# Performance work log

Hardware: AMD Instinct MI355X
Metric: run time of the kernel (lower is better)

Reference implementation:

```python
import jax, jax.numpy as jnp
import numpy as np

B, L = 1024, 4096        # cycles x timesteps
CC = 3                   # SC channels (SC[...,2:3] = nominal capacity)
XC = 2 + CC              # p_net input: [SOC, T, SC...]
# bounds from params['a123'] for (R_1, 1/R_1C_1, OCV-U, -M_H, K_H)
LB = jnp.array([0.005, 0.025, 0.1, 0.0, 0.002], dtype=jnp.float32)
UB = jnp.array([0.02, 0.07, 1.0, 0.055, 0.025], dtype=jnp.float32)


def setup_inputs() -> dict:
    key = jax.random.key(0)
    ks = jax.random.split(key, 10)
    t = jnp.broadcast_to(jnp.arange(L, dtype=jnp.float32), (B, L))  # monotone time
    I = 1.0 + 0.1 * jax.random.normal(ks[0], (B, L))  # current, bounded away from 0 (IR_estim divides by I)
    T = jax.random.normal(ks[1], (B, L))              # temperature
    dummy = jax.random.normal(ks[2], (B, L))          # unused column 3
    SOC = jax.random.uniform(ks[3], (B, L))
    X = jnp.stack([t, I, T, dummy, SOC], axis=-1)     # [B, L, 5]
    SC = jax.random.uniform(ks[4], (B, CC), minval=0.5, maxval=1.5)
    std = 0.1  # init_network_weights: normal(0, 0.1), zero bias
    pW1 = std * jax.random.normal(ks[5], (XC, 2 * XC))
    pb1 = jnp.zeros((2 * XC,), jnp.float32)
    pW2 = std * jax.random.normal(ks[6], (2 * XC, 5))
    pb2 = jnp.zeros((5,), jnp.float32)
    rW1 = std * jax.random.normal(ks[7], (XC, 1))
    rb1 = jnp.zeros((1,), jnp.float32)
    rW2 = std * jax.random.normal(ks[8], (1, 1))
    rb2 = jnp.zeros((1,), jnp.float32)
    return dict(X=X, SC=SC, pW1=pW1, pb1=pb1, pW2=pW2, pb2=pb2,
                rW1=rW1, rb1=rb1, rW2=rW2, rb2=rb2)


def reference(X, SC, pW1, pb1, pW2, pb2, rW1, rb1, rW2, rb2):
    t = X[..., 0:1]
    I = X[..., 1:2]
    T = X[..., 2:3]
    SOC = X[..., 4:]
    sc_b = jnp.broadcast_to(SC[:, None, :], (X.shape[0], X.shape[1], SC.shape[-1]))
    x = jnp.concatenate([SOC, T, sc_b], axis=-1)                 # [B, L, XC]
    p = jax.nn.softplus(x @ pW1 + pb1) @ pW2 + pb2               # [B, L, 5]
    theta = LB + (UB - LB) * jax.nn.sigmoid(0.01 * p)
    R_1 = theta[..., 0:1]
    RC_r = theta[..., 1:2]
    OCV_U = theta[..., 2:3]
    M_Hn = theta[..., 3:4]   # -M_H
    K_H = theta[..., 4:5]
    r = jax.nn.softplus(x[:, 0, :] @ rW1 + rb1) @ rW2 + rb2      # [B, 1]
    R_s_init = SC[..., 2:3] * (1.0 + r)
    U_H0 = jnp.zeros((X.shape[0], 1), X.dtype)
    U_10 = -OCV_U[:, 0, :] - U_H0 - I[:, 0, :] * R_s_init
    y0 = jnp.concatenate([U_H0, U_10], axis=-1)                  # [B, 2]

    dt = jnp.swapaxes(t[:, 1:, :] - t[:, :-1, :], 0, 1)          # [L-1, B, 1]
    tm = lambda a: jnp.swapaxes(a[:, :-1, :], 0, 1)              # step inputs use X_ode[:, i]
    scan_in = (dt, tm(I), tm(R_1), tm(RC_r), tm(M_Hn), tm(K_H))

    def step(y, inp):  # explicit Euler, IRODEFunc derivative
        dt_i, I_i, R1_i, RC_i, MH_i, KH_i = inp
        U_H = y[..., 0:1]
        U_1 = y[..., 1:2]
        dU_H = -KH_i * I_i * (-MH_i - U_H)
        dU_1 = RC_i * (R1_i * I_i - U_1)
        y = y + dt_i * jnp.concatenate([dU_H, dU_1], axis=-1)
        return y, y

    _, ys = jax.lax.scan(step, y0, scan_in)                      # [L-1, B, 2]
    voltages = jnp.concatenate([y0[None], ys], axis=0)           # [L, B, 2]
    voltages = jnp.swapaxes(voltages, 0, 1)                      # [B, L, 2]
    U_H = voltages[..., 0:1]
    U_1 = voltages[..., 1:2]
    IR_estim = jnp.nanmean((-OCV_U - U_H - U_1) / I, axis=-2)    # [B, 1]
    return IR_estim
```

## Files before the change

### kernel.cpp

```cpp
#include <hip/hip_runtime.h>

#define NB   1024
#define NL   4096
#define TPB  256
#define HALF 2048
#define SPT  8

#define WS_BASE 256
#define WS_PART 16640

typedef float v2f __attribute__((ext_vector_type(2)));

__device__ __forceinline__ float rfl(float x) {
    return __uint_as_float(__builtin_amdgcn_readfirstlane(__float_as_uint(x)));
}
__device__ __forceinline__ float fast_rcp(float x) { return __builtin_amdgcn_rcpf(x); }
__device__ __forceinline__ float fexp2(float x) { return __builtin_amdgcn_exp2f(x); }
__device__ __forceinline__ float flog2(float x) { return __builtin_amdgcn_logf(x); }

#define L2E 1.44269504088896340736f
#define LN2 0.69314718055994530942f

__global__ void __launch_bounds__(256) onenet_prep(
    const float* __restrict__ X,   const float* __restrict__ SC,
    const float* __restrict__ pW1, const float* __restrict__ pb1,
    const float* __restrict__ pW2, const float* __restrict__ pb2,
    const float* __restrict__ rW1, const float* __restrict__ rb1,
    const float* __restrict__ rW2, const float* __restrict__ rb2,
    float* __restrict__ ws)
{
    const int gid = blockIdx.x * 256 + threadIdx.x;
    if (gid < NB) {
        float sc0 = SC[gid * 3 + 0], sc1 = SC[gid * 3 + 1], sc2 = SC[gid * 3 + 2];
        float* bp = ws + WS_BASE + gid * 16;
#pragma unroll
        for (int j = 0; j < 10; ++j) {
            float base = fmaf(sc0, pW1[20 + j],
                         fmaf(sc1, pW1[30 + j],
                         fmaf(sc2, pW1[40 + j], pb1[j])));
            bp[j] = L2E * base;
        }
        const float* x0 = X + (size_t)gid * NL * 5;
        float T0 = x0[2], SOC0 = x0[4];
        float u = rb1[0];
        u = fmaf(SOC0, rW1[0], u);
        u = fmaf(T0,   rW1[1], u);
        u = fmaf(sc0,  rW1[2], u);
        u = fmaf(sc1,  rW1[3], u);
        u = fmaf(sc2,  rW1[4], u);
        float sp = LN2 * flog2(1.0f + fexp2(L2E * u));
        float r  = fmaf(sp, rW2[0], rb2[0]);
        bp[10] = sc2 * (1.0f + r);
    }
    if (blockIdx.x == 0 && threadIdx.x < 75) {
        const int t = threadIdx.x;
        const float LBv[5]   = {0.005f, 0.025f, 0.1f, 0.0f, 0.002f};
        const float UBLB[5]  = {0.015f, 0.045f, 0.9f, 0.055f, 0.023f};
        float v;
        if (t < 20) {
            v = L2E * pW1[t];
        } else if (t < 70) {
            int k = (t - 20) % 5;
            v = LN2 * 0.0025f * UBLB[k] * pW2[t - 20];
        } else {
            int k = t - 70;
            v = LBv[k] + UBLB[k] * fmaf(0.0025f, pb2[k], 0.5f);
        }
        ws[t] = v;
    }
}

__global__ void __launch_bounds__(TPB) onenet_main(
    const float* __restrict__ X, float* __restrict__ ws)
{
    const int bid  = blockIdx.x;
    const int row  = bid >> 1;
    const int half = bid & 1;
    const int tid  = threadIdx.x;
    const int lane = tid & 63;
    const int w    = tid >> 6;

    float W1S[10], W1T[10], BASE[10], V4[10];
    v2f V01[10], V23[10], AL01, AL23;
    float AL4;
#pragma unroll
    for (int j = 0; j < 10; ++j) W1S[j] = rfl(ws[j]);
#pragma unroll
    for (int j = 0; j < 10; ++j) W1T[j] = rfl(ws[10 + j]);
#pragma unroll
    for (int j = 0; j < 10; ++j) {
        V01[j].x = rfl(ws[20 + 5 * j + 0]);
        V01[j].y = rfl(ws[20 + 5 * j + 1]);
        V23[j].x = rfl(ws[20 + 5 * j + 2]);
        V23[j].y = rfl(ws[20 + 5 * j + 3]);
        V4[j]    = rfl(ws[20 + 5 * j + 4]);
    }
    AL01.x = rfl(ws[70]); AL01.y = rfl(ws[71]);
    AL23.x = rfl(ws[72]); AL23.y = rfl(ws[73]);
    AL4    = rfl(ws[74]);
    {
        const float* bp = ws + WS_BASE + row * 16;
#pragma unroll
        for (int j = 0; j < 10; ++j) BASE[j] = rfl(bp[j]);
    }

    const float* xp = X + ((size_t)row * NL + (size_t)(half * HALF + tid * SPT)) * 5;
    const bool lastthr = (half == 1) && (tid == TPB - 1);

    v2f a  = {1.f, 1.f}, b  = {0.f, 0.f};
    v2f cS = {0.f, 0.f}, dS = {0.f, 0.f};
    float oacc = 0.f, OCV0 = 0.f, I0 = 0.f;

#pragma unroll
    for (int ch = 0; ch < 2; ++ch) {
        float f[20];
#pragma unroll
        for (int q = 0; q < 5; ++q) {
            float4 v4 = reinterpret_cast<const float4*>(xp)[ch * 5 + q];
            f[4 * q + 0] = v4.x; f[4 * q + 1] = v4.y;
            f[4 * q + 2] = v4.z; f[4 * q + 3] = v4.w;
        }
        float tn = (ch == 0) ? xp[20] : (lastthr ? 0.f : xp[40]);

#pragma unroll
        for (int i = 0; i < 4; ++i) {
            float tt = f[5 * i + 0];
            float Ii = f[5 * i + 1];
            float Tt = f[5 * i + 2];
            float SS = f[5 * i + 4];
            float tnx = (i < 3) ? f[5 * i + 5] : tn;
            float dt  = tnx - tt;
            float inv = fast_rcp(Ii);

            v2f t01 = AL01, t23 = AL23;
            float t4 = AL4;
#pragma unroll
            for (int j = 0; j < 10; ++j) {
                float pre = fmaf(SS, W1S[j], fmaf(Tt, W1T[j], BASE[j]));
                float lam = flog2(1.0f + fexp2(pre));
                v2f lam2 = {lam, lam};
                t01 = lam2 * V01[j] + t01;
                t23 = lam2 * V23[j] + t23;
                t4  = fmaf(lam, V4[j], t4);
            }
            oacc = fmaf(-t23.x, inv, oacc);
            if (ch == 0 && i == 0) { OCV0 = t23.x; I0 = Ii; }

            bool lastl = lastthr && (ch == 1) && (i == 3);
            float g  = lastl ? 0.f : dt * t4 * Ii;
            float hh = lastl ? 0.f : dt * t01.y;
            v2f sv, bv, iv;
            sv.x = 1.f + g;      sv.y = 1.f - hh;
            bv.x = g * t23.y;    bv.y = hh * t01.x * Ii;
            iv.x = inv;          iv.y = inv;

            cS = iv * a + cS;
            dS = iv * b + dS;
            b  = sv * b + bv;
            a  = sv * a;
        }
    }

#pragma unroll
    for (int off = 1; off < 64; off <<= 1) {
        v2f a2, b2, c2, d2;
        a2.x = __shfl_down(a.x, off);  a2.y = __shfl_down(a.y, off);
        b2.x = __shfl_down(b.x, off);  b2.y = __shfl_down(b.y, off);
        c2.x = __shfl_down(cS.x, off); c2.y = __shfl_down(cS.y, off);
        d2.x = __shfl_down(dS.x, off); d2.y = __shfl_down(dS.y, off);
        float o2 = __shfl_down(oacc, off);
        v2f nb = a2 * b + b2;
        v2f nc = c2 * a + cS;
        v2f nd = (dS + d2) + c2 * b;
        a = a2 * a; b = nb; cS = nc; dS = nd;
        oacc += o2;
    }

    __shared__ float red[TPB / 64][9];
    if (lane == 0) {
        red[w][0] = a.x;  red[w][1] = a.y;
        red[w][2] = b.x;  red[w][3] = b.y;
        red[w][4] = cS.x; red[w][5] = cS.y;
        red[w][6] = dS.x; red[w][7] = dS.y;
        red[w][8] = oacc;
    }
    __syncthreads();

    if (tid == 0) {
#pragma unroll
        for (int k = 1; k < TPB / 64; ++k) {
            v2f ak, bk, ck, dk;
            ak.x = red[k][0]; ak.y = red[k][1];
            bk.x = red[k][2]; bk.y = red[k][3];
            ck.x = red[k][4]; ck.y = red[k][5];
            dk.x = red[k][6]; dk.y = red[k][7];
            v2f nb = ak * b + bk;
            v2f nc = ck * a + cS;
            v2f nd = (dS + dk) + ck * b;
            a = ak * a; b = nb; cS = nc; dS = nd;
            oacc += red[k][8];
        }
        float* pw = ws + WS_PART + (row * 2 + half) * 12;
        pw[0] = a.x;  pw[1] = b.x;  pw[2] = cS.x; pw[3] = dS.x;
        pw[4] = a.y;  pw[5] = b.y;  pw[6] = cS.y; pw[7] = dS.y;
        pw[8] = oacc;
        if (half == 0) { pw[9] = OCV0; pw[10] = I0; }
    }
}

__global__ void __launch_bounds__(256) onenet_final(
    const float* __restrict__ ws, float* __restrict__ out)
{
    const int row = blockIdx.x * 256 + threadIdx.x;
    if (row >= NB) return;
    const float* q0 = ws + WS_PART + row * 24;
    const float* q1 = q0 + 12;
    float DH = q0[3] + q1[3] + q1[2] * q0[1];
    float C1 = fmaf(q1[6], q0[4], q0[6]);
    float D1 = q0[7] + q1[7] + q1[6] * q0[5];
    float O  = q0[8] + q1[8];
    float OCV0 = q0[9], I0 = q0[10];
    float Rs   = ws[WS_BASE + row * 16 + 10];
    float U10  = -OCV0 - I0 * Rs;
    float S1   = fmaf(C1, U10, D1);
    out[row] = (O - DH - S1) * (1.0f / 4096.0f);
}

extern "C" void kernel_launch(void* const* d_in, const int* in_sizes, int n_in,
                              void* d_out, int out_size, void* d_ws, size_t ws_size,
                              hipStream_t stream) {
    const float* X   = (const float*)d_in[0];
    const float* SC  = (const float*)d_in[1];
    const float* pW1 = (const float*)d_in[2];
    const float* pb1 = (const float*)d_in[3];
    const float* pW2 = (const float*)d_in[4];
    const float* pb2 = (const float*)d_in[5];
    const float* rW1 = (const float*)d_in[6];
    const float* rb1 = (const float*)d_in[7];
    const float* rW2 = (const float*)d_in[8];
    const float* rb2 = (const float*)d_in[9];
    float* out = (float*)d_out;
    float* ws  = (float*)d_ws;

    onenet_prep<<<NB / 256, 256, 0, stream>>>(X, SC, pW1, pb1, pW2, pb2,
                                              rW1, rb1, rW2, rb2, ws);
    onenet_main<<<NB * 2, TPB, 0, stream>>>(X, ws);
    onenet_final<<<NB / 256, 256, 0, stream>>>(ws, out);
}
```

Baseline: 140.9 us.

## Split each row into four quarter blocks and combine partial scans in final kernel

Each row's time axis is now split across four blocks instead of two, each thread handling 4 timesteps instead of 8, with a single load chunk. The final kernel composes four affine-scan partials instead of two. The readfirstlane wrappers on weight loads are removed, and the last-step zeroing is replaced by reusing the thread's own time so dt becomes zero. This aims to raise parallelism and latency hiding, at the cost of more blocks and more per-block weight-loading and reduction overhead.

```diff
diff --git a/kernel.cpp b/kernel.cpp
--- a/kernel.cpp
+++ b/kernel.cpp
@@ -3,17 +3,14 @@
 #define NB   1024
 #define NL   4096
 #define TPB  256
-#define HALF 2048
-#define SPT  8
+#define QSTEP 1024
+#define SPT  4
 
 #define WS_BASE 256
 #define WS_PART 16640
 
 typedef float v2f __attribute__((ext_vector_type(2)));
 
-__device__ __forceinline__ float rfl(float x) {
-    return __uint_as_float(__builtin_amdgcn_readfirstlane(__float_as_uint(x)));
-}
 __device__ __forceinline__ float fast_rcp(float x) { return __builtin_amdgcn_rcpf(x); }
 __device__ __forceinline__ float fexp2(float x) { return __builtin_amdgcn_exp2f(x); }
 __device__ __forceinline__ float flog2(float x) { return __builtin_amdgcn_logf(x); }
@@ -74,8 +71,8 @@
     const float* __restrict__ X, float* __restrict__ ws)
 {
     const int bid  = blockIdx.x;
-    const int row  = bid >> 1;
-    const int half = bid & 1;
+    const int row  = bid >> 2;
+    const int q    = bid & 3;
     const int tid  = threadIdx.x;
     const int lane = tid & 63;
     const int w    = tid >> 6;
@@ -84,81 +81,70 @@
     v2f V01[10], V23[10], AL01, AL23;
     float AL4;
 #pragma unroll
-    for (int j = 0; j < 10; ++j) W1S[j] = rfl(ws[j]);
-#pragma unroll
-    for (int j = 0; j < 10; ++j) W1T[j] = rfl(ws[10 + j]);
+    for (int j = 0; j < 10; ++j) W1S[j] = ws[j];
+#pragma unroll
+    for (int j = 0; j < 10; ++j) W1T[j] = ws[10 + j];
 #pragma unroll
     for (int j = 0; j < 10; ++j) {
-        V01[j].x = rfl(ws[20 + 5 * j + 0]);
-        V01[j].y = rfl(ws[20 + 5 * j + 1]);
-        V23[j].x = rfl(ws[20 + 5 * j + 2]);
-        V23[j].y = rfl(ws[20 + 5 * j + 3]);
-        V4[j]    = rfl(ws[20 + 5 * j + 4]);
-    }
-    AL01.x = rfl(ws[70]); AL01.y = rfl(ws[71]);
-    AL23.x = rfl(ws[72]); AL23.y = rfl(ws[73]);
-    AL4    = rfl(ws[74]);
+        V01[j].x = ws[20 + 5 * j + 0];
+        V01[j].y = ws[20 + 5 * j + 1];
+        V23[j].x = ws[20 + 5 * j + 2];
+        V23[j].y = ws[20 + 5 * j + 3];
+        V4[j]    = ws[20 + 5 * j + 4];
+    }
+    AL01.x = ws[70]; AL01.y = ws[71];
+    AL23.x = ws[72]; AL23.y = ws[73];
+    AL4    = ws[74];
     {
         const float* bp = ws + WS_BASE + row * 16;
 #pragma unroll
-        for (int j = 0; j < 10; ++j) BASE[j] = rfl(bp[j]);
-    }
-
-    const float* xp = X + ((size_t)row * NL + (size_t)(half * HALF + tid * SPT)) * 5;
-    const bool lastthr = (half == 1) && (tid == TPB - 1);
-
-    v2f a  = {1.f, 1.f}, b  = {0.f, 0.f};
-    v2f cS = {0.f, 0.f}, dS = {0.f, 0.f};
+        for (int j = 0; j < 10; ++j) BASE[j] = bp[j];
+    }
+
+    const float* xp = X + ((size_t)row * NL + (size_t)(q * QSTEP + tid * SPT)) * 5;
+
+    float f[20];
+#pragma unroll
+    for (int k = 0; k < 5; ++k)
+        *(float4*)&f[4 * k] = reinterpret_cast<const float4*>(xp)[k];
+    float tn = (q == 3 && tid == TPB - 1) ? f[15] : xp[20];
+
+    v2f a = {1.f, 1.f}, b = {0.f, 0.f}, cS = {0.f, 0.f}, dS = {0.f, 0.f};
     float oacc = 0.f, OCV0 = 0.f, I0 = 0.f;
 
 #pragma unroll
-    for (int ch = 0; ch < 2; ++ch) {
-        float f[20];
-#pragma unroll
-        for (int q = 0; q < 5; ++q) {
-            float4 v4 = reinterpret_cast<const float4*>(xp)[ch * 5 + q];
-            f[4 * q + 0] = v4.x; f[4 * q + 1] = v4.y;
-            f[4 * q + 2] = v4.z; f[4 * q + 3] = v4.w;
-        }
-        float tn = (ch == 0) ? xp[20] : (lastthr ? 0.f : xp[40]);
-
-#pragma unroll
-        for (int i = 0; i < 4; ++i) {
-            float tt = f[5 * i + 0];
-            float Ii = f[5 * i + 1];
-            float Tt = f[5 * i + 2];
-            float SS = f[5 * i + 4];
-            float tnx = (i < 3) ? f[5 * i + 5] : tn;
-            float dt  = tnx - tt;
-            float inv = fast_rcp(Ii);
-
-            v2f t01 = AL01, t23 = AL23;
-            float t4 = AL4;
-#pragma unroll
-            for (int j = 0; j < 10; ++j) {
-                float pre = fmaf(SS, W1S[j], fmaf(Tt, W1T[j], BASE[j]));
-                float lam = flog2(1.0f + fexp2(pre));
-                v2f lam2 = {lam, lam};
-                t01 = lam2 * V01[j] + t01;
-                t23 = lam2 * V23[j] + t23;
-                t4  = fmaf(lam, V4[j], t4);
-            }
-            oacc = fmaf(-t23.x, inv, oacc);
-            if (ch == 0 && i == 0) { OCV0 = t23.x; I0 = Ii; }
-
-            bool lastl = lastthr && (ch == 1) && (i == 3);
-            float g  = lastl ? 0.f : dt * t4 * Ii;
-            float hh = lastl ? 0.f : dt * t01.y;
-            v2f sv, bv, iv;
-            sv.x = 1.f + g;      sv.y = 1.f - hh;
-            bv.x = g * t23.y;    bv.y = hh * t01.x * Ii;
-            iv.x = inv;          iv.y = inv;
-
-            cS = iv * a + cS;
-            dS = iv * b + dS;
-            b  = sv * b + bv;
-            a  = sv * a;
-        }
+    for (int i = 0; i < SPT; ++i) {
+        float tt = f[5 * i + 0];
+        float Ii = f[5 * i + 1];
+        float Tt = f[5 * i + 2];
+        float SS = f[5 * i + 4];
+        float tnx = (i < SPT - 1) ? f[5 * i + 5] : tn;
+        float dt  = tnx - tt;
+        float inv = fast_rcp(Ii);
+
+        v2f t01 = AL01, t23 = AL23;
+        float t4 = AL4;
+#pragma unroll
+        for (int j = 0; j < 10; ++j) {
+            float pre = fmaf(SS, W1S[j], fmaf(Tt, W1T[j], BASE[j]));
+            float lam = flog2(1.0f + fexp2(pre));
+            v2f lam2 = {lam, lam};
+            t01 = lam2 * V01[j] + t01;
+            t23 = lam2 * V23[j] + t23;
+            t4  = fmaf(lam, V4[j], t4);
+        }
+        oacc = fmaf(-t23.x, inv, oacc);
+        if (i == 0) { OCV0 = t23.x; I0 = Ii; }
+
+        float g  = dt * t4 * Ii;
+        float hh = dt * t01.y;
+        v2f sv = {1.f + g, 1.f - hh};
+        v2f bv = {g * t23.y, hh * t01.x * Ii};
+        v2f iv = {inv, inv};
+        cS = iv * a + cS;
+        dS = iv * b + dS;
+        b  = sv * b + bv;
+        a  = sv * a;
     }
 
 #pragma unroll
@@ -200,11 +186,11 @@
             a = ak * a; b = nb; cS = nc; dS = nd;
             oacc += red[k][8];
         }
-        float* pw = ws + WS_PART + (row * 2 + half) * 12;
+        float* pw = ws + WS_PART + (size_t)bid * 12;
         pw[0] = a.x;  pw[1] = b.x;  pw[2] = cS.x; pw[3] = dS.x;
         pw[4] = a.y;  pw[5] = b.y;  pw[6] = cS.y; pw[7] = dS.y;
         pw[8] = oacc;
-        if (half == 0) { pw[9] = OCV0; pw[10] = I0; }
+        if (q == 0) { pw[9] = OCV0; pw[10] = I0; }
     }
 }
 
@@ -213,17 +199,34 @@
 {
     const int row = blockIdx.x * 256 + threadIdx.x;
     if (row >= NB) return;
-    const float* q0 = ws + WS_PART + row * 24;
-    const float* q1 = q0 + 12;
-    float DH = q0[3] + q1[3] + q1[2] * q0[1];
-    float C1 = fmaf(q1[6], q0[4], q0[6]);
-    float D1 = q0[7] + q1[7] + q1[6] * q0[5];
-    float O  = q0[8] + q1[8];
-    float OCV0 = q0[9], I0 = q0[10];
-    float Rs   = ws[WS_BASE + row * 16 + 10];
-    float U10  = -OCV0 - I0 * Rs;
-    float S1   = fmaf(C1, U10, D1);
-    out[row] = (O - DH - S1) * (1.0f / 4096.0f);
+    const float* p0 = ws + WS_PART + (size_t)row * 48;
+
+    v2f a, b, cS, dS;
+    a.x  = p0[0]; a.y  = p0[4];
+    b.x  = p0[1]; b.y  = p0[5];
+    cS.x = p0[2]; cS.y = p0[6];
+    dS.x = p0[3]; dS.y = p0[7];
+    float O = p0[8];
+    float OCV0 = p0[9], I0 = p0[10];
+#pragma unroll
+    for (int k = 1; k < 4; ++k) {
+        const float* pk = p0 + k * 12;
+        v2f ak, bk, ck, dk;
+        ak.x = pk[0]; ak.y = pk[4];
+        bk.x = pk[1]; bk.y = pk[5];
+        ck.x = pk[2]; ck.y = pk[6];
+        dk.x = pk[3]; dk.y = pk[7];
+        v2f nb = ak * b + bk;
+        v2f nc = ck * a + cS;
+        v2f nd = (dS + dk) + ck * b;
+        a = ak * a; b = nb; cS = nc; dS = nd;
+        O += pk[8];
+    }
+    float Rs  = ws[WS_BASE + row * 16 + 10];
+    float U10 = -OCV0 - I0 * Rs;
+    float SH  = dS.x;
+    float S1  = fmaf(cS.y, U10, dS.y);
+    out[row] = (O - SH - S1) * (1.0f / 4096.0f);
 }
 
 extern "C" void kernel_launch(void* const* d_in, const int* in_sizes, int n_in,
@@ -244,6 +247,6 @@
 
     onenet_prep<<<NB / 256, 256, 0, stream>>>(X, SC, pW1, pb1, pW2, pb2,
                                               rW1, rb1, rW2, rb2, ws);
-    onenet_main<<<NB * 2, TPB, 0, stream>>>(X, ws);
+    onenet_main<<<NB * 4, TPB, 0, stream>>>(X, ws);
     onenet_final<<<NB / 256, 256, 0, stream>>>(ws, out);
 }
```

New measurement: 140.8 us. About the same (-0.1%).
